# Kernel tuning notes

Measured on AMD Instinct MI355X. Metric: run time of the kernel, lower is better.

The kernel has to match this reference:

```python
import jax, jax.numpy as jnp
import numpy as np

N, E, F_IN, HID, NCLS, K, D = 50000, 800000, 128, 64, 16, 3, 2
EPS = 1e-15


def gmm_conv(x, src, dst, edge_attr, g, mu, sigma, root, bias):
    # x: [N, Fin]; g: [Fin, K*M]; mu, sigma: [K, D]; root: [Fin, M]; bias: [M]
    M = g.shape[1] // K
    h = x @ g                                        # [N, K*M]
    hj = h[src].reshape(-1, K, M)                    # edge gather [E, K, M]
    diff = edge_attr[:, None, :] - mu[None, :, :]    # [E, K, D]
    gauss = jnp.exp((-0.5 * diff * diff / (EPS + sigma[None] ** 2)).sum(-1))  # [E, K]
    msg = (hj * gauss[:, :, None]).sum(axis=1)       # [E, M]
    agg = jax.ops.segment_sum(msg, dst, num_segments=N)                  # scatter-add
    deg = jax.ops.segment_sum(jnp.ones(msg.shape[0], x.dtype), dst, num_segments=N)
    agg = agg / jnp.maximum(deg, 1.0)[:, None]       # mean aggregation
    return agg + x @ root + bias


def setup_inputs() -> dict:
    key = jax.random.key(0)
    ks = jax.random.split(key, 13)
    x = jax.random.normal(ks[0], (N, F_IN), jnp.float32)
    edge_index = jax.random.randint(ks[1], (2, E), 0, N, dtype=jnp.int64)
    edge_attr = jax.random.uniform(ks[2], (E, D), jnp.float32)
    s1 = 1.0 / np.sqrt(F_IN)
    s2 = 1.0 / np.sqrt(HID)
    return {
        "x": x,
        "edge_index": edge_index,
        "edge_attr": edge_attr,
        "g1": jax.random.normal(ks[3], (F_IN, K * HID), jnp.float32) * s1,
        "mu1": jax.random.normal(ks[4], (K, D), jnp.float32),
        "sigma1": jnp.ones((K, D), jnp.float32),
        "root1": jax.random.normal(ks[5], (F_IN, HID), jnp.float32) * s1,
        "b1": jnp.zeros((HID,), jnp.float32),
        "g2": jax.random.normal(ks[6], (HID, K * NCLS), jnp.float32) * s2,
        "mu2": jax.random.normal(ks[7], (K, D), jnp.float32),
        "sigma2": jnp.ones((K, D), jnp.float32),
        "root2": jax.random.normal(ks[8], (HID, NCLS), jnp.float32) * s2,
        "b2": jnp.zeros((NCLS,), jnp.float32),
    }


def reference(x, edge_index, edge_attr, g1, mu1, sigma1, root1, b1, g2, mu2, sigma2, root2, b2):
    # eval mode: dropout is identity
    src, dst = edge_index[0], edge_index[1]
    h = gmm_conv(x, src, dst, edge_attr, g1, mu1, sigma1, root1, b1)
    h = jax.nn.elu(h)
    out = gmm_conv(h, src, dst, edge_attr, g2, mu2, sigma2, root2, b2)
    return jax.nn.log_softmax(out, axis=1)
```

## Files before the change

### kernel.cpp

```cpp
#include <hip/hip_runtime.h>
#include <hip/hip_fp16.h>

#define EPS 1e-15f
#define BKT_SHIFT 7
#define BKT_SIZE 128
#define NBKT_MAX 512

typedef _Float16 v8h __attribute__((ext_vector_type(8)));
typedef float v4f __attribute__((ext_vector_type(4)));
typedef float v2f __attribute__((ext_vector_type(2)));

#if __has_builtin(__builtin_amdgcn_cvt_pk_f32_fp8) && __has_builtin(__builtin_amdgcn_cvt_pk_fp8_f32)
#define FP8_HW 1
#else
#define FP8_HW 0
#endif

__device__ __forceinline__ unsigned char f32_to_fp8(float v) {
#if FP8_HW
    int r = __builtin_amdgcn_cvt_pk_fp8_f32(v, v, 0, false);
    return (unsigned char)(r & 0xFF);
#else
    __half h = __float2half(v);
    unsigned short u; __builtin_memcpy(&u, &h, 2);
    int s = (u >> 15) << 7;
    int a = (u & 0x7FFF) + 0x40;
    if (a < (9 << 10)) return (unsigned char)s;
    int t = (a >> 7) - 64;
    if (t > 126) t = 126;
    return (unsigned char)(s | t);
#endif
}

__device__ __forceinline__ float2 fp8x2_to_f32(unsigned short w) {
#if FP8_HW
    v2f r = __builtin_amdgcn_cvt_pk_f32_fp8((int)w, false);
    return make_float2(r.x, r.y);
#else
    int b0 = w & 0xFF, b1 = w >> 8;
    unsigned short h0 = (unsigned short)((((b0 & 0x7F) + 64) << 7) | ((b0 & 0x80) << 8));
    unsigned short h1 = (unsigned short)((((b1 & 0x7F) + 64) << 7) | ((b1 & 0x80) << 8));
    __half x0, x1;
    __builtin_memcpy(&x0, &h0, 2);
    __builtin_memcpy(&x1, &h1, 2);
    return make_float2(__half2float(x0), __half2float(x1));
#endif
}

__device__ __forceinline__ int load_idx(const int* __restrict__ ei, int is64, int pos) {
    return is64 ? ei[(size_t)2 * pos] : ei[pos];
}

__device__ __forceinline__ int h2_as_int(__half2 h) {
    int w; __builtin_memcpy(&w, &h, 4); return w;
}
__device__ __forceinline__ __half2 int_as_h2(int w) {
    __half2 h; __builtin_memcpy(&h, &w, 4); return h;
}

__global__ void detect_kernel(const int* __restrict__ ei, int* __restrict__ flag,
                              int* __restrict__ bcnt, int nbkt) {
    __shared__ int any_odd;
    if (threadIdx.x == 0) any_odd = 0;
    __syncthreads();
    for (int u = threadIdx.x; u < nbkt; u += 256) bcnt[u] = 0;
    if (ei[2 * threadIdx.x + 1] != 0) atomicOr(&any_odd, 1);
    __syncthreads();
    if (threadIdx.x == 0) *flag = any_odd ? 0 : 1;
}

__global__ __launch_bounds__(256) void bhist_kernel(
    const int* __restrict__ ei, const int* __restrict__ flag,
    int* __restrict__ bcnt, int E, int nbkt) {
    __shared__ int cnt[NBKT_MAX];
    int t = threadIdx.x;
    for (int u = t; u < nbkt; u += 256) cnt[u] = 0;
    __syncthreads();
    int is64 = *flag;
    int e0 = blockIdx.x * 4096;
#pragma unroll
    for (int i = 0; i < 16; ++i) {
        int e = e0 + i * 256 + t;
        if (e < E) atomicAdd(&cnt[load_idx(ei, is64, E + e) >> BKT_SHIFT], 1);
    }
    __syncthreads();
    for (int u = t; u < nbkt; u += 256)
        if (cnt[u]) atomicAdd(&bcnt[u], cnt[u]);
}

__global__ void bscan_kernel(const int* __restrict__ bcnt, int* __restrict__ bbase,
                             int* __restrict__ bcursor, int* __restrict__ rowptrN,
                             int nbkt, int E) {
    __shared__ int s[512];
    int t = threadIdx.x;
    int v = (t < nbkt) ? bcnt[t] : 0;
    s[t] = v;
    __syncthreads();
    for (int o = 1; o < 512; o <<= 1) {
        int u = (t >= o) ? s[t - o] : 0;
        __syncthreads();
        s[t] += u;
        __syncthreads();
    }
    if (t < nbkt) { int ex = s[t] - v; bbase[t] = ex; bcursor[t] = ex; }
    if (t == 0) { bbase[nbkt] = E; *rowptrN = E; }
}

__global__ __launch_bounds__(1024) void pass1_kernel(
    const int* __restrict__ ei, const int* __restrict__ flag,
    const float2* __restrict__ ea, int* __restrict__ bcursor,
    int4* __restrict__ staging, int E, int nbkt) {
    __shared__ int lcnt[NBKT_MAX];
    __shared__ int lcur[NBKT_MAX];
    int t = threadIdx.x;
    if (t < nbkt) lcnt[t] = 0;
    __syncthreads();
    int is64 = *flag;
    int e0 = blockIdx.x * 8192;
    int eend = min(e0 + 8192, E);

    for (int e = e0 + t; e < eend; e += 1024)
        atomicAdd(&lcnt[load_idx(ei, is64, E + e) >> BKT_SHIFT], 1);
    __syncthreads();

    if (t < nbkt) {
        int c = lcnt[t];
        lcur[t] = c ? atomicAdd(&bcursor[t], c) : 0;
    }
    __syncthreads();

    for (int e = e0 + t; e < eend; e += 1024) {
        int src = load_idx(ei, is64, e);
        int dst = load_idx(ei, is64, E + e);
        float2 a = ea[e];
        int pos = atomicAdd(&lcur[dst >> BKT_SHIFT], 1);
        staging[pos] = make_int4(src, dst,
                                 __float_as_int(a.x), __float_as_int(a.y));
    }
}

__global__ __launch_bounds__(256) void pass2_kernel(
    const int4* __restrict__ staging, const int* __restrict__ bbase,
    const float* __restrict__ mu1, const float* __restrict__ sg1,
    const float* __restrict__ mu2, const float* __restrict__ sg2,
    int4* __restrict__ rec, int* __restrict__ rowptr, int N) {
    __shared__ int lcnt[BKT_SIZE];
    __shared__ int ssc[BKT_SIZE];
    __shared__ int lcur[BKT_SIZE];
    int b = blockIdx.x;
    int node0 = b << BKT_SHIFT;
    int t = threadIdx.x;
    int beg = bbase[b], end = bbase[b + 1];

    if (t < BKT_SIZE) lcnt[t] = 0;
    __syncthreads();
    for (int j = beg + t; j < end; j += 256)
        atomicAdd(&lcnt[staging[j].y & (BKT_SIZE - 1)], 1);
    __syncthreads();
    int v = (t < BKT_SIZE) ? lcnt[t] : 0;
    if (t < BKT_SIZE) ssc[t] = v;
    __syncthreads();
    for (int o = 1; o < BKT_SIZE; o <<= 1) {
        int u = (t < BKT_SIZE && t >= o) ? ssc[t - o] : 0;
        __syncthreads();
        if (t < BKT_SIZE) ssc[t] += u;
        __syncthreads();
    }
    if (t < BKT_SIZE) {
        int excl = beg + ssc[t] - v;
        lcur[t] = excl;
        if (node0 + t < N) rowptr[node0 + t] = excl;
    }
    __syncthreads();

    float m1x[3], m1y[3], i1x[3], i1y[3], m2x[3], m2y[3], i2x[3], i2y[3];
#pragma unroll
    for (int k = 0; k < 3; ++k) {
        m1x[k] = mu1[2 * k]; m1y[k] = mu1[2 * k + 1];
        float s0 = sg1[2 * k], s1 = sg1[2 * k + 1];
        i1x[k] = -0.5f / (EPS + s0 * s0); i1y[k] = -0.5f / (EPS + s1 * s1);
        m2x[k] = mu2[2 * k]; m2y[k] = mu2[2 * k + 1];
        s0 = sg2[2 * k]; s1 = sg2[2 * k + 1];
        i2x[k] = -0.5f / (EPS + s0 * s0); i2y[k] = -0.5f / (EPS + s1 * s1);
    }

    for (int j = beg + t; j < end; j += 256) {
        int4 p = staging[j];
        float ax = __int_as_float(p.z), ay = __int_as_float(p.w);
        float g1v[3], g2v[3];
#pragma unroll
        for (int k = 0; k < 3; ++k) {
            float d0 = ax - m1x[k], d1 = ay - m1y[k];
            g1v[k] = __expf(d0 * d0 * i1x[k] + d1 * d1 * i1y[k]);
            d0 = ax - m2x[k]; d1 = ay - m2y[k];
            g2v[k] = __expf(d0 * d0 * i2x[k] + d1 * d1 * i2y[k]);
        }
        int pos = atomicAdd(&lcur[p.y & (BKT_SIZE - 1)], 1);
        int4 r;
        r.x = p.x;
        r.y = h2_as_int(__floats2half2_rn(g1v[0], g1v[1]));
        r.z = h2_as_int(__floats2half2_rn(g1v[2], g2v[0]));
        r.w = h2_as_int(__floats2half2_rn(g2v[1], g2v[2]));
        rec[pos] = r;
    }
}

__global__ void bprep_kernel(const float* __restrict__ g1, const float* __restrict__ r1,
                             __half* __restrict__ Bprep) {
    int gid = blockIdx.x * 256 + threadIdx.x;
    if (gid >= 32768) return;
    int fi = gid >> 9;
    int lane = (gid >> 3) & 63;
    int i = gid & 7;
    int ks = fi & 3, cb = fi >> 2;
    int k = ks * 32 + (lane >> 4) * 8 + i;
    int c = cb * 16 + (lane & 15);
    float v = (c < 192) ? g1[k * 192 + c] : r1[k * 64 + (c - 192)];
    Bprep[gid] = __float2half(v);
}

__global__ __launch_bounds__(256) void gemm1_mfma(
    const float* __restrict__ A, const __half* __restrict__ Bprep,
    unsigned char* __restrict__ hw1k, __half* __restrict__ hw1r, int M) {
    __shared__ char a_lds[64 * 256];
    int row0 = blockIdx.x * 64;
    int tid = threadIdx.x;
    int wid = tid >> 6, lane = tid & 63;

    const float4* xf4 = reinterpret_cast<const float4*>(A);
#pragma unroll
    for (int j = 0; j < 8; ++j) {
        int g = j * 256 + tid;
        int r = g >> 5, c = g & 31;
        int gr = row0 + r;
        float4 f = (gr < M) ? xf4[(size_t)gr * 32 + c]
                            : make_float4(0.f, 0.f, 0.f, 0.f);
        int2 v;
        v.x = h2_as_int(__floats2half2_rn(f.x, f.y));
        v.y = h2_as_int(__floats2half2_rn(f.z, f.w));
        int byte = r * 256 + c * 8;
        byte ^= (r & 7) << 4;
        *reinterpret_cast<int2*>(&a_lds[byte]) = v;
    }

    v8h bf[2][4];
#pragma unroll
    for (int cf = 0; cf < 2; ++cf)
#pragma unroll
        for (int ks = 0; ks < 4; ++ks) {
            int cb = blockIdx.y * 8 + wid * 2 + cf;
            int fi = cb * 4 + ks;
            bf[cf][ks] = *reinterpret_cast<const v8h*>(Bprep + (size_t)fi * 512 + lane * 8);
        }

    __syncthreads();

    v4f acc[4][2] = {};
#pragma unroll
    for (int ks = 0; ks < 4; ++ks) {
        v8h af[4];
#pragma unroll
        for (int rf = 0; rf < 4; ++rf) {
            int r = rf * 16 + (lane & 15);
            int byte = r * 256 + ks * 64 + (lane >> 4) * 16;
            byte ^= (r & 7) << 4;
            af[rf] = *reinterpret_cast<const v8h*>(&a_lds[byte]);
        }
#pragma unroll
        for (int rf = 0; rf < 4; ++rf)
#pragma unroll
            for (int cf = 0; cf < 2; ++cf)
                acc[rf][cf] = __builtin_amdgcn_mfma_f32_16x16x32_f16(
                    af[rf], bf[cf][ks], acc[rf][cf], 0, 0, 0);
    }

#pragma unroll
    for (int rf = 0; rf < 4; ++rf)
#pragma unroll
        for (int cf = 0; cf < 2; ++cf) {
            int gc = blockIdx.y * 128 + wid * 32 + cf * 16 + (lane & 15);
#pragma unroll
            for (int i = 0; i < 4; ++i) {
                int gr = row0 + rf * 16 + (lane >> 4) * 4 + i;
                if (gr < M) {
                    float val = acc[rf][cf][i];
                    if (gc < 192)
                        hw1k[(size_t)gr * 192 + gc] = f32_to_fp8(val);
                    else
                        hw1r[(size_t)gr * 64 + (gc - 192)] = __float2half(val);
                }
            }
        }
}

template<int K, int TN, int TC, int C1, int C2>
__global__ __launch_bounds__(256) void gemm_cat(
    const float* __restrict__ A, const float* __restrict__ W1,
    const float* __restrict__ W2, __half* __restrict__ Cout, int nrows) {
    constexpr int NT = TN / 8;
    constexpr int CT = TC / 4;
    static_assert(NT * CT == 256, "bad tile");
    constexpr int COLS = C1 + C2;
    __shared__ float xs[TN][K + 4];

    int row0 = blockIdx.x * TN;
    int col0 = blockIdx.y * TC;

    constexpr int NV = TN * (K / 4);
    for (int id = threadIdx.x; id < NV; id += 256) {
        int r  = id / (K / 4);
        int k4 = id % (K / 4);
        int gr = row0 + r;
        float4 v = make_float4(0.f, 0.f, 0.f, 0.f);
        if (gr < nrows) v = reinterpret_cast<const float4*>(A + (size_t)gr * K)[k4];
        *reinterpret_cast<float4*>(&xs[r][4 * k4]) = v;
    }
    __syncthreads();

    int ct = threadIdx.x % CT;
    int nt = threadIdx.x / CT;
    int c0 = col0 + ct * 4;

    const float* wp;
    int wstride;
    if (c0 < C1) { wp = W1 + c0;        wstride = C1; }
    else         { wp = W2 + (c0 - C1); wstride = C2; }

    float acc[8][4] = {};
#pragma unroll 4
    for (int k = 0; k < K; ++k) {
        float4 w = *reinterpret_cast<const float4*>(wp + (size_t)k * wstride);
        float xr[8];
#pragma unroll
        for (int i = 0; i < 8; ++i) xr[i] = xs[nt * 8 + i][k];
#pragma unroll
        for (int i = 0; i < 8; ++i) {
            acc[i][0] += xr[i] * w.x;
            acc[i][1] += xr[i] * w.y;
            acc[i][2] += xr[i] * w.z;
            acc[i][3] += xr[i] * w.w;
        }
    }

#pragma unroll
    for (int i = 0; i < 8; ++i) {
        int gr = row0 + nt * 8 + i;
        if (gr < nrows) {
            __half2* p = reinterpret_cast<__half2*>(Cout + (size_t)gr * COLS + c0);
            p[0] = __floats2half2_rn(acc[i][0], acc[i][1]);
            p[1] = __floats2half2_rn(acc[i][2], acc[i][3]);
        }
    }
}

__global__ __launch_bounds__(256) void agg1_kernel(
    const int4* __restrict__ rec, const int* __restrict__ rowptr,
    const unsigned char* __restrict__ hw1k, const __half* __restrict__ hw1r,
    const float* __restrict__ b1, float* __restrict__ h2, int N) {
    int node = (blockIdx.x * 256 + threadIdx.x) >> 5;
    int l = threadIdx.x & 31;
    if (node >= N) return;
    int beg = rowptr[node], end = rowptr[node + 1];
    float ax0 = 0.f, ay0 = 0.f, ax1 = 0.f, ay1 = 0.f;
    int j = beg;
    for (; j + 3 < end; j += 4) {
        int4 r0 = rec[j], r1 = rec[j + 1], r2 = rec[j + 2], r3 = rec[j + 3];
        const unsigned short* p0 = reinterpret_cast<const unsigned short*>(
            hw1k + (size_t)r0.x * 192);
        const unsigned short* p1 = reinterpret_cast<const unsigned short*>(
            hw1k + (size_t)r1.x * 192);
        const unsigned short* p2 = reinterpret_cast<const unsigned short*>(
            hw1k + (size_t)r2.x * 192);
        const unsigned short* p3 = reinterpret_cast<const unsigned short*>(
            hw1k + (size_t)r3.x * 192);
        unsigned short w00 = p0[l], w01 = p0[32 + l], w02 = p0[64 + l];
        unsigned short w10 = p1[l], w11 = p1[32 + l], w12 = p1[64 + l];
        unsigned short w20 = p2[l], w21 = p2[32 + l], w22 = p2[64 + l];
        unsigned short w30 = p3[l], w31 = p3[32 + l], w32 = p3[64 + l];
        __half2 ha0 = int_as_h2(r0.y), hb0 = int_as_h2(r0.z);
        __half2 ha1 = int_as_h2(r1.y), hb1 = int_as_h2(r1.z);
        __half2 ha2 = int_as_h2(r2.y), hb2 = int_as_h2(r2.z);
        __half2 ha3 = int_as_h2(r3.y), hb3 = int_as_h2(r3.z);
        {
            float g0 = __low2float(ha0), g1 = __high2float(ha0), g2 = __low2float(hb0);
            float2 a = fp8x2_to_f32(w00), b = fp8x2_to_f32(w01), c = fp8x2_to_f32(w02);
            ax0 += g0 * a.x + g1 * b.x + g2 * c.x;
            ay0 += g0 * a.y + g1 * b.y + g2 * c.y;
        }
        {
            float g0 = __low2float(ha1), g1 = __high2float(ha1), g2 = __low2float(hb1);
            float2 a = fp8x2_to_f32(w10), b = fp8x2_to_f32(w11), c = fp8x2_to_f32(w12);
            ax1 += g0 * a.x + g1 * b.x + g2 * c.x;
            ay1 += g0 * a.y + g1 * b.y + g2 * c.y;
        }
        {
            float g0 = __low2float(ha2), g1 = __high2float(ha2), g2 = __low2float(hb2);
            float2 a = fp8x2_to_f32(w20), b = fp8x2_to_f32(w21), c = fp8x2_to_f32(w22);
            ax0 += g0 * a.x + g1 * b.x + g2 * c.x;
            ay0 += g0 * a.y + g1 * b.y + g2 * c.y;
        }
        {
            float g0 = __low2float(ha3), g1 = __high2float(ha3), g2 = __low2float(hb3);
            float2 a = fp8x2_to_f32(w30), b = fp8x2_to_f32(w31), c = fp8x2_to_f32(w32);
            ax1 += g0 * a.x + g1 * b.x + g2 * c.x;
            ay1 += g0 * a.y + g1 * b.y + g2 * c.y;
        }
    }
    for (; j < end; ++j) {
        int4 r0 = rec[j];
        __half2 ha0 = int_as_h2(r0.y), hb0 = int_as_h2(r0.z);
        float g0 = __low2float(ha0), g1 = __high2float(ha0), g2 = __low2float(hb0);
        const unsigned short* p0 = reinterpret_cast<const unsigned short*>(
            hw1k + (size_t)r0.x * 192);
        float2 a = fp8x2_to_f32(p0[l]);
        float2 b = fp8x2_to_f32(p0[32 + l]);
        float2 c = fp8x2_to_f32(p0[64 + l]);
        ax0 += g0 * a.x + g1 * b.x + g2 * c.x;
        ay0 += g0 * a.y + g1 * b.y + g2 * c.y;
    }
    float d = fmaxf((float)(end - beg), 1.0f);
    float2 root = __half22float2(
        reinterpret_cast<const __half2*>(hw1r + (size_t)node * 64)[l]);
    float2 bb = reinterpret_cast<const float2*>(b1)[l];
    float v0 = (ax0 + ax1) / d + root.x + bb.x;
    float v1 = (ay0 + ay1) / d + root.y + bb.y;
    float2 o;
    o.x = v0 > 0.f ? v0 : expm1f(v0);
    o.y = v1 > 0.f ? v1 : expm1f(v1);
    reinterpret_cast<float2*>(h2 + (size_t)node * 64)[l] = o;
}

__global__ __launch_bounds__(256) void agg2_kernel(
    const int4* __restrict__ rec, const int* __restrict__ rowptr,
    const __half* __restrict__ hw2h, const float* __restrict__ b2,
    float* __restrict__ out, int N) {
    int node = (blockIdx.x * 256 + threadIdx.x) >> 3;
    int l = threadIdx.x & 7;
    if (node >= N) return;
    int beg = rowptr[node], end = rowptr[node + 1];
    float ax = 0.f, ay = 0.f;
    for (int j = beg; j < end; ++j) {
        int4 r = rec[j];
        __half2 hb = int_as_h2(r.z), hc = int_as_h2(r.w);
        float g0 = __high2float(hb), g1 = __low2float(hc), g2 = __high2float(hc);
        const __half2* p = reinterpret_cast<const __half2*>(hw2h + (size_t)r.x * 64);
        float2 f0 = __half22float2(p[l]);
        float2 f1 = __half22float2(p[8 + l]);
        float2 f2 = __half22float2(p[16 + l]);
        ax += g0 * f0.x + g1 * f1.x + g2 * f2.x;
        ay += g0 * f0.y + g1 * f1.y + g2 * f2.y;
    }
    float d = fmaxf((float)(end - beg), 1.0f);
    float2 root = __half22float2(
        reinterpret_cast<const __half2*>(hw2h + (size_t)node * 64 + 48)[l]);
    float2 bb = reinterpret_cast<const float2*>(b2)[l];
    float v0 = ax / d + root.x + bb.x;
    float v1 = ay / d + root.y + bb.y;

    float mx = fmaxf(v0, v1);
#pragma unroll
    for (int off = 4; off >= 1; off >>= 1) mx = fmaxf(mx, __shfl_xor(mx, off, 8));
    float s = __expf(v0 - mx) + __expf(v1 - mx);
#pragma unroll
    for (int off = 4; off >= 1; off >>= 1) s += __shfl_xor(s, off, 8);
    float ls = __logf(s);
    float2 o = make_float2(v0 - mx - ls, v1 - mx - ls);
    reinterpret_cast<float2*>(out + (size_t)node * 16)[l] = o;
}

extern "C" void kernel_launch(void* const* d_in, const int* in_sizes, int n_in,
                              void* d_out, int out_size, void* d_ws, size_t ws_size,
                              hipStream_t stream) {
    const float* x   = (const float*)d_in[0];
    const int*   ei  = (const int*)d_in[1];
    const float* ea  = (const float*)d_in[2];
    const float* g1  = (const float*)d_in[3];
    const float* mu1 = (const float*)d_in[4];
    const float* sg1 = (const float*)d_in[5];
    const float* r1  = (const float*)d_in[6];
    const float* b1  = (const float*)d_in[7];
    const float* g2  = (const float*)d_in[8];
    const float* mu2 = (const float*)d_in[9];
    const float* sg2 = (const float*)d_in[10];
    const float* r2  = (const float*)d_in[11];
    const float* b2  = (const float*)d_in[12];

    const int N = in_sizes[0] / 128;
    const int E = in_sizes[2] / 2;
    const int nbkt = (N + BKT_SIZE - 1) >> BKT_SHIFT;

    unsigned char* hw1k = (unsigned char*)d_ws;
    __half* hw1r = (__half*)(hw1k + (size_t)N * 192);
    float*  h2   = (float*)(hw1r + (size_t)N * 64);
    __half* hw2h = (__half*)(h2 + (size_t)N * 64);
    int4*   rec  = (int4*)(hw2h + (size_t)N * 64);
    int4*   staging = rec + E;
    __half* Bprep = (__half*)(staging + E);
    int*    rowptr  = (int*)(Bprep + 32768);
    int*    bcnt    = rowptr + N + 1;
    int*    bbase   = bcnt + nbkt;
    int*    bcursor = bbase + nbkt + 1;
    int*    flag    = bcursor + nbkt;

    detect_kernel<<<1, 256, 0, stream>>>(ei, flag, bcnt, nbkt);
    bhist_kernel<<<(E + 4095) / 4096, 256, 0, stream>>>(ei, flag, bcnt, E, nbkt);
    bscan_kernel<<<1, 512, 0, stream>>>(bcnt, bbase, bcursor, rowptr + N, nbkt, E);

    pass1_kernel<<<(E + 8191) / 8192, 1024, 0, stream>>>(
        ei, flag, (const float2*)ea, bcursor, staging, E, nbkt);
    pass2_kernel<<<nbkt, 256, 0, stream>>>(
        staging, bbase, mu1, sg1, mu2, sg2, rec, rowptr, N);

    bprep_kernel<<<128, 256, 0, stream>>>(g1, r1, Bprep);
    gemm1_mfma<<<dim3((N + 63) / 64, 2), 256, 0, stream>>>(x, Bprep, hw1k, hw1r, N);

    agg1_kernel<<<((size_t)N * 32 + 255) / 256, 256, 0, stream>>>(
        rec, rowptr, hw1k, hw1r, b1, h2, N);

    gemm_cat<64, 128, 64, 48, 16>
        <<<dim3((N + 127) / 128, 1), 256, 0, stream>>>(h2, g2, r2, hw2h, N);

    agg2_kernel<<<((size_t)N * 8 + 255) / 256, 256, 0, stream>>>(
        rec, rowptr, hw2h, b2, (float*)d_out, N);
}
```

Baseline: 135.9 us.

## Fuse layer-2 dense transform into layer-1 aggregation kernel via LDS

The layer-1 aggregation kernel now keeps each block's 8 ELU-activated node rows in shared memory and multiplies them by the concatenated g2/root2 weights, which are also staged in LDS. It writes the fp16 layer-2 features directly. This removes the fp32 h2 intermediate round trip through global memory and one kernel launch. In exchange, every block reloads the 16KB weight matrix into LDS and adds a block barrier, and the per-node matvec is done with scalar FMAs, which may lower occupancy.

Result: faster. 133.1 us (-2.1%).

```diff
diff --git a/kernel.cpp b/kernel.cpp
--- a/kernel.cpp
+++ b/kernel.cpp
@@ -293,84 +293,37 @@
         }
 }
 
-template<int K, int TN, int TC, int C1, int C2>
-__global__ __launch_bounds__(256) void gemm_cat(
-    const float* __restrict__ A, const float* __restrict__ W1,
-    const float* __restrict__ W2, __half* __restrict__ Cout, int nrows) {
-    constexpr int NT = TN / 8;
-    constexpr int CT = TC / 4;
-    static_assert(NT * CT == 256, "bad tile");
-    constexpr int COLS = C1 + C2;
-    __shared__ float xs[TN][K + 4];
-
-    int row0 = blockIdx.x * TN;
-    int col0 = blockIdx.y * TC;
-
-    constexpr int NV = TN * (K / 4);
-    for (int id = threadIdx.x; id < NV; id += 256) {
-        int r  = id / (K / 4);
-        int k4 = id % (K / 4);
-        int gr = row0 + r;
-        float4 v = make_float4(0.f, 0.f, 0.f, 0.f);
-        if (gr < nrows) v = reinterpret_cast<const float4*>(A + (size_t)gr * K)[k4];
-        *reinterpret_cast<float4*>(&xs[r][4 * k4]) = v;
-    }
-    __syncthreads();
-
-    int ct = threadIdx.x % CT;
-    int nt = threadIdx.x / CT;
-    int c0 = col0 + ct * 4;
-
-    const float* wp;
-    int wstride;
-    if (c0 < C1) { wp = W1 + c0;        wstride = C1; }
-    else         { wp = W2 + (c0 - C1); wstride = C2; }
-
-    float acc[8][4] = {};
-#pragma unroll 4
-    for (int k = 0; k < K; ++k) {
-        float4 w = *reinterpret_cast<const float4*>(wp + (size_t)k * wstride);
-        float xr[8];
-#pragma unroll
-        for (int i = 0; i < 8; ++i) xr[i] = xs[nt * 8 + i][k];
-#pragma unroll
-        for (int i = 0; i < 8; ++i) {
-            acc[i][0] += xr[i] * w.x;
-            acc[i][1] += xr[i] * w.y;
-            acc[i][2] += xr[i] * w.z;
-            acc[i][3] += xr[i] * w.w;
-        }
-    }
-
-#pragma unroll
-    for (int i = 0; i < 8; ++i) {
-        int gr = row0 + nt * 8 + i;
-        if (gr < nrows) {
-            __half2* p = reinterpret_cast<__half2*>(Cout + (size_t)gr * COLS + c0);
-            p[0] = __floats2half2_rn(acc[i][0], acc[i][1]);
-            p[1] = __floats2half2_rn(acc[i][2], acc[i][3]);
-        }
-    }
-}
-
-__global__ __launch_bounds__(256) void agg1_kernel(
+__global__ __launch_bounds__(256) void agg1_fused(
     const int4* __restrict__ rec, const int* __restrict__ rowptr,
     const unsigned char* __restrict__ hw1k, const __half* __restrict__ hw1r,
-    const float* __restrict__ b1, float* __restrict__ h2, int N) {
-    int node = (blockIdx.x * 256 + threadIdx.x) >> 5;
-    int l = threadIdx.x & 31;
-    if (node >= N) return;
-    int beg = rowptr[node], end = rowptr[node + 1];
+    const float* __restrict__ b1, const float* __restrict__ g2,
+    const float* __restrict__ r2, __half* __restrict__ hw2h, int N) {
+    __shared__ float Wlds[64][64];
+    __shared__ float h2s[8][64];
+    int t = threadIdx.x;
+
+    for (int i = t; i < 4096; i += 256) {
+        int k = i >> 6, c = i & 63;
+        Wlds[k][c] = (c < 48) ? g2[k * 48 + c] : r2[k * 16 + (c - 48)];
+    }
+
+    int node = (blockIdx.x * 256 + t) >> 5;
+    int nl = (t >> 5) & 7;
+    int l = t & 31;
+    bool active = node < N;
+
     float ax0 = 0.f, ay0 = 0.f, ax1 = 0.f, ay1 = 0.f;
+    int beg = 0, end = 0;
+    if (active) { beg = rowptr[node]; end = rowptr[node + 1]; }
     int j = beg;
     for (; j + 3 < end; j += 4) {
-        int4 r0 = rec[j], r1 = rec[j + 1], r2 = rec[j + 2], r3 = rec[j + 3];
+        int4 r0 = rec[j], r1 = rec[j + 1], r2v = rec[j + 2], r3 = rec[j + 3];
         const unsigned short* p0 = reinterpret_cast<const unsigned short*>(
             hw1k + (size_t)r0.x * 192);
         const unsigned short* p1 = reinterpret_cast<const unsigned short*>(
             hw1k + (size_t)r1.x * 192);
         const unsigned short* p2 = reinterpret_cast<const unsigned short*>(
-            hw1k + (size_t)r2.x * 192);
+            hw1k + (size_t)r2v.x * 192);
         const unsigned short* p3 = reinterpret_cast<const unsigned short*>(
             hw1k + (size_t)r3.x * 192);
         unsigned short w00 = p0[l], w01 = p0[32 + l], w02 = p0[64 + l];
@@ -379,55 +332,69 @@
         unsigned short w30 = p3[l], w31 = p3[32 + l], w32 = p3[64 + l];
         __half2 ha0 = int_as_h2(r0.y), hb0 = int_as_h2(r0.z);
         __half2 ha1 = int_as_h2(r1.y), hb1 = int_as_h2(r1.z);
-        __half2 ha2 = int_as_h2(r2.y), hb2 = int_as_h2(r2.z);
+        __half2 ha2 = int_as_h2(r2v.y), hb2 = int_as_h2(r2v.z);
         __half2 ha3 = int_as_h2(r3.y), hb3 = int_as_h2(r3.z);
         {
-            float g0 = __low2float(ha0), g1 = __high2float(ha0), g2 = __low2float(hb0);
+            float g0 = __low2float(ha0), g1 = __high2float(ha0), gg2 = __low2float(hb0);
             float2 a = fp8x2_to_f32(w00), b = fp8x2_to_f32(w01), c = fp8x2_to_f32(w02);
-            ax0 += g0 * a.x + g1 * b.x + g2 * c.x;
-            ay0 += g0 * a.y + g1 * b.y + g2 * c.y;
+            ax0 += g0 * a.x + g1 * b.x + gg2 * c.x;
+            ay0 += g0 * a.y + g1 * b.y + gg2 * c.y;
         }
         {
-            float g0 = __low2float(ha1), g1 = __high2float(ha1), g2 = __low2float(hb1);
+            float g0 = __low2float(ha1), g1 = __high2float(ha1), gg2 = __low2float(hb1);
             float2 a = fp8x2_to_f32(w10), b = fp8x2_to_f32(w11), c = fp8x2_to_f32(w12);
-            ax1 += g0 * a.x + g1 * b.x + g2 * c.x;
-            ay1 += g0 * a.y + g1 * b.y + g2 * c.y;
+            ax1 += g0 * a.x + g1 * b.x + gg2 * c.x;
+            ay1 += g0 * a.y + g1 * b.y + gg2 * c.y;
         }
         {
-            float g0 = __low2float(ha2), g1 = __high2float(ha2), g2 = __low2float(hb2);
+            float g0 = __low2float(ha2), g1 = __high2float(ha2), gg2 = __low2float(hb2);
             float2 a = fp8x2_to_f32(w20), b = fp8x2_to_f32(w21), c = fp8x2_to_f32(w22);
-            ax0 += g0 * a.x + g1 * b.x + g2 * c.x;
-            ay0 += g0 * a.y + g1 * b.y + g2 * c.y;
+            ax0 += g0 * a.x + g1 * b.x + gg2 * c.x;
+            ay0 += g0 * a.y + g1 * b.y + gg2 * c.y;
         }
         {
-            float g0 = __low2float(ha3), g1 = __high2float(ha3), g2 = __low2float(hb3);
+            float g0 = __low2float(ha3), g1 = __high2float(ha3), gg2 = __low2float(hb3);
             float2 a = fp8x2_to_f32(w30), b = fp8x2_to_f32(w31), c = fp8x2_to_f32(w32);
-            ax1 += g0 * a.x + g1 * b.x + g2 * c.x;
-            ay1 += g0 * a.y + g1 * b.y + g2 * c.y;
+            ax1 += g0 * a.x + g1 * b.x + gg2 * c.x;
+            ay1 += g0 * a.y + g1 * b.y + gg2 * c.y;
         }
     }
     for (; j < end; ++j) {
         int4 r0 = rec[j];
         __half2 ha0 = int_as_h2(r0.y), hb0 = int_as_h2(r0.z);
-        float g0 = __low2float(ha0), g1 = __high2float(ha0), g2 = __low2float(hb0);
+        float g0 = __low2float(ha0), g1 = __high2float(ha0), gg2 = __low2float(hb0);
         const unsigned short* p0 = reinterpret_cast<const unsigned short*>(
             hw1k + (size_t)r0.x * 192);
         float2 a = fp8x2_to_f32(p0[l]);
         float2 b = fp8x2_to_f32(p0[32 + l]);
         float2 c = fp8x2_to_f32(p0[64 + l]);
-        ax0 += g0 * a.x + g1 * b.x + g2 * c.x;
-        ay0 += g0 * a.y + g1 * b.y + g2 * c.y;
-    }
-    float d = fmaxf((float)(end - beg), 1.0f);
-    float2 root = __half22float2(
-        reinterpret_cast<const __half2*>(hw1r + (size_t)node * 64)[l]);
-    float2 bb = reinterpret_cast<const float2*>(b1)[l];
-    float v0 = (ax0 + ax1) / d + root.x + bb.x;
-    float v1 = (ay0 + ay1) / d + root.y + bb.y;
-    float2 o;
-    o.x = v0 > 0.f ? v0 : expm1f(v0);
-    o.y = v1 > 0.f ? v1 : expm1f(v1);
-    reinterpret_cast<float2*>(h2 + (size_t)node * 64)[l] = o;
+        ax0 += g0 * a.x + g1 * b.x + gg2 * c.x;
+        ay0 += g0 * a.y + g1 * b.y + gg2 * c.y;
+    }
+    if (active) {
+        float d = fmaxf((float)(end - beg), 1.0f);
+        float2 root = __half22float2(
+            reinterpret_cast<const __half2*>(hw1r + (size_t)node * 64)[l]);
+        float2 bb = reinterpret_cast<const float2*>(b1)[l];
+        float v0 = (ax0 + ax1) / d + root.x + bb.x;
+        float v1 = (ay0 + ay1) / d + root.y + bb.y;
+        h2s[nl][2 * l]     = v0 > 0.f ? v0 : expm1f(v0);
+        h2s[nl][2 * l + 1] = v1 > 0.f ? v1 : expm1f(v1);
+    }
+    __syncthreads();
+
+    if (active) {
+        float acc0 = 0.f, acc1 = 0.f;
+#pragma unroll 8
+        for (int k = 0; k < 64; ++k) {
+            float hv = h2s[nl][k];
+            float2 w = *reinterpret_cast<const float2*>(&Wlds[k][2 * l]);
+            acc0 += hv * w.x;
+            acc1 += hv * w.y;
+        }
+        reinterpret_cast<__half2*>(hw2h)[(size_t)node * 32 + l] =
+            __floats2half2_rn(acc0, acc1);
+    }
 }
 
 __global__ __launch_bounds__(256) void agg2_kernel(
@@ -491,8 +458,7 @@
 
     unsigned char* hw1k = (unsigned char*)d_ws;
     __half* hw1r = (__half*)(hw1k + (size_t)N * 192);
-    float*  h2   = (float*)(hw1r + (size_t)N * 64);
-    __half* hw2h = (__half*)(h2 + (size_t)N * 64);
+    __half* hw2h = (__half*)(hw1r + (size_t)N * 64);
     int4*   rec  = (int4*)(hw2h + (size_t)N * 64);
     int4*   staging = rec + E;
     __half* Bprep = (__half*)(staging + E);
@@ -514,11 +480,8 @@
     bprep_kernel<<<128, 256, 0, stream>>>(g1, r1, Bprep);
     gemm1_mfma<<<dim3((N + 63) / 64, 2), 256, 0, stream>>>(x, Bprep, hw1k, hw1r, N);
 
-    agg1_kernel<<<((size_t)N * 32 + 255) / 256, 256, 0, stream>>>(
-        rec, rowptr, hw1k, hw1r, b1, h2, N);
-
-    gemm_cat<64, 128, 64, 48, 16>
-        <<<dim3((N + 127) / 128, 1), 256, 0, stream>>>(h2, g2, r2, hw2h, N);
+    agg1_fused<<<((size_t)N * 32 + 255) / 256, 256, 0, stream>>>(
+        rec, rowptr, hw1k, hw1r, b1, g2, r2, hw2h, N);
 
     agg2_kernel<<<((size_t)N * 8 + 255) / 256, 256, 0, stream>>>(
         rec, rowptr, hw2h, b2, (float*)d_out, N);
```
